# Kernel tuning notes

Hardware: AMD Instinct MI355X
Metric: run time of the kernel (lower is better)

The kernel has to match this reference:

```python
import jax, jax.numpy as jnp
import numpy as np

N = 50000      # nodes
E = 800000     # edges
F_IN = 128     # input_dim
H = 4          # GAT heads
C = 32         # hidden_dim (per head)
HC = H * C     # 128, concat GAT output
NG = 64        # graphs in batch
OUT = 10       # classes


def _gat_conv(x, src, dst, W, att_src, att_dst, bias):
    # PyG GATConv (concat=True, add_self_loops=True, negative_slope=0.2)
    n = x.shape[0]
    h = (x @ W).reshape(n, H, -1)                      # [N,H,C]
    a_s = (h * att_src).sum(-1)                        # [N,H]
    a_d = (h * att_dst).sum(-1)                        # [N,H]
    loop = jnp.arange(n)
    s = jnp.concatenate([src, loop])                   # self-loops appended
    d = jnp.concatenate([dst, loop])
    e = jax.nn.leaky_relu(a_s[s] + a_d[d], 0.2)        # [E+N,H]
    m = jax.ops.segment_max(e, d, num_segments=n)
    e = jnp.exp(e - m[d])
    z = jax.ops.segment_sum(e, d, num_segments=n)
    alpha = e / (z[d] + 1e-16)                         # edge softmax per dst,head
    out = jax.ops.segment_sum(h[s] * alpha[..., None], d, num_segments=n)
    return out.reshape(n, -1) + bias                   # [N,H*C]


def setup_inputs() -> dict:
    key = jax.random.key(0)
    ks = jax.random.split(key, 20)
    g = lambda k, shp, fan: jax.random.normal(k, shp, jnp.float32) / np.sqrt(fan)
    inp = {
        'x': jax.random.normal(ks[0], (N, F_IN), jnp.float32),
        'edge_index': jax.random.randint(ks[1], (2, E), 0, N),
        'batch': jnp.sort(jax.random.randint(ks[2], (N,), 0, NG)),
        # GATConv 1: F_IN -> H*C
        'W1': g(ks[3], (F_IN, HC), F_IN),
        'as1': g(ks[4], (H, C), C), 'ad1': g(ks[5], (H, C), C),
        'b1': jnp.zeros((HC,), jnp.float32),
        # GATConv 2: H*C -> H*C
        'W2': g(ks[6], (HC, HC), HC),
        'as2': g(ks[7], (H, C), C), 'ad2': g(ks[8], (H, C), C),
        'b2': jnp.zeros((HC,), jnp.float32),
        # GraphConv: H*C -> C  (lin_rel has bias, lin_root does not)
        'W3r': g(ks[9], (HC, C), HC), 'W3l': g(ks[10], (HC, C), HC),
        'b3': jnp.zeros((C,), jnp.float32),
        # SAGEConv: C -> C (mean aggr; lin_l has bias, lin_r does not)
        'W4l': g(ks[11], (C, C), C), 'b4l': jnp.zeros((C,), jnp.float32),
        'W4r': g(ks[12], (C, C), C),
        # MLP head
        'Wf1': g(ks[13], (C, C), C), 'bf1': jnp.zeros((C,), jnp.float32),
        'Wf2': g(ks[14], (C, OUT), C), 'bf2': jnp.zeros((OUT,), jnp.float32),
    }
    return inp


def reference(x, edge_index, batch, W1, as1, ad1, b1, W2, as2, ad2, b2,
              W3r, W3l, b3, W4l, b4l, W4r, Wf1, bf1, Wf2, bf2):
    src, dst = edge_index[0], edge_index[1]
    relu = jax.nn.relu
    n = x.shape[0]
    # GAT layers (dropout is identity in eval)
    x = relu(_gat_conv(x, src, dst, W1, as1, ad1, b1))
    x = relu(_gat_conv(x, src, dst, W2, as2, ad2, b2))
    # GraphConv: lin_rel(sum_neighbors) + lin_root(x)
    agg = jax.ops.segment_sum(x[src], dst, num_segments=n)
    x = relu(agg @ W3r + b3 + x @ W3l)
    # SAGEConv: lin_l(mean_neighbors) + lin_r(x)
    deg = jax.ops.segment_sum(jnp.ones((src.shape[0],), x.dtype), dst, num_segments=n)
    mean = jax.ops.segment_sum(x[src], dst, num_segments=n) / jnp.maximum(deg, 1.0)[:, None]
    x = relu(mean @ W4l + b4l + x @ W4r)
    # global mean pool over graphs
    cnt = jax.ops.segment_sum(jnp.ones((n,), x.dtype), batch, num_segments=NG)
    gpool = jax.ops.segment_sum(x, batch, num_segments=NG) / jnp.maximum(cnt, 1.0)[:, None]
    gpool = relu(gpool @ Wf1 + bf1)
    return gpool @ Wf2 + bf2
```

## Files before the change

kernel.cpp:

```cpp
#include <hip/hip_runtime.h>
#include <hip/hip_bf16.h>
#include <type_traits>


typedef __bf16 v8bf __attribute__((ext_vector_type(8)));
typedef float  v4f  __attribute__((ext_vector_type(4)));
typedef float  v2f  __attribute__((ext_vector_type(2)));

__device__ __forceinline__ float lrelu(float x) { return x > 0.f ? x : 0.2f * x; }

__device__ __forceinline__ unsigned short f2bf(float f) {
    unsigned u = __float_as_uint(f);
    unsigned r = (u + 0x7FFF + ((u >> 16) & 1)) >> 16;
    return (unsigned short)r;
}
__device__ __forceinline__ float bfbits2f(unsigned short u) {
    return __uint_as_float((unsigned)u << 16);
}
__device__ __forceinline__ float bflo(int v) { return __uint_as_float((unsigned)v << 16); }
__device__ __forceinline__ float bfhi(int v) { return __uint_as_float((unsigned)v & 0xffff0000u); }
__device__ __forceinline__ v2f up2(int v) {
    v2f r; r.x = bflo(v); r.y = bfhi(v); return r;
}
__device__ __forceinline__ int packbf2(float a, float b) {
    return (int)f2bf(a) | ((int)f2bf(b) << 16);
}


__global__ __launch_bounds__(256) void bucket_hist(const int* __restrict__ dst,
                                                   int* __restrict__ bcount,
                                                   int E, int nbuck) {
    __shared__ int hist[256];
    int t = threadIdx.x;
    for (int i = t; i < nbuck; i += 256) hist[i] = 0;
    __syncthreads();
    int base = blockIdx.x * 4096;
    #pragma unroll
    for (int k = 0; k < 16; ++k) {
        int e = base + k * 256 + t;
        if (e < E) atomicAdd(&hist[dst[e] >> 8], 1);
    }
    __syncthreads();
    for (int i = t; i < nbuck; i += 256) {
        int c = hist[i];
        if (c) atomicAdd(&bcount[i], c);
    }
}

__global__ __launch_bounds__(256) void scan_convert(
    const int* __restrict__ bcount, int* __restrict__ bbase, int* __restrict__ gcursor,
    int nbuck, int E, int* __restrict__ rowptr, int n,
    const float* __restrict__ W1, const float* __restrict__ W2,
    const float* __restrict__ W3r, const float* __restrict__ W3l,
    const float* __restrict__ as1, const float* __restrict__ ad1,
    const float* __restrict__ as2, const float* __restrict__ ad2,
    __hip_bfloat16* __restrict__ W1t, __hip_bfloat16* __restrict__ W2t,
    __hip_bfloat16* __restrict__ W3rt, __hip_bfloat16* __restrict__ W3lt)
{
    int t = threadIdx.x;
    if (blockIdx.x == 0) {
        __shared__ int red[256];
        int v = (t < nbuck) ? bcount[t] : 0;
        red[t] = v;
        __syncthreads();
        for (int off = 1; off < 256; off <<= 1) {
            int u = (t >= off) ? red[t - off] : 0;
            __syncthreads();
            red[t] += u;
            __syncthreads();
        }
        int ex = red[t] - v;
        if (t < nbuck) { bbase[t] = ex; gcursor[t] = ex; }
        if (t == 0) { bbase[nbuck] = E; rowptr[n] = E; }
        return;
    }
    int b = blockIdx.x - 1;
    int i = b * 256 + t;
    {
        int k = i >> 7, c = i & 127;
        *(unsigned short*)&W1t[c * 128 + k] = f2bf(W1[i]);
        *(unsigned short*)&W2t[c * 128 + k] = f2bf(W2[i]);
    }
    if (i < 4096) {
        int k = i >> 5, c = i & 31;
        *(unsigned short*)&W3rt[c * 128 + k] = f2bf(W3r[i]);
        *(unsigned short*)&W3lt[c * 128 + k] = f2bf(W3l[i]);
    }
    if (b == 0) {
        for (int u = t; u < 512; u += 256) {
            int k = u & 127, hd = u >> 7;
            float vs1 = 0.f, vd1 = 0.f, vs2 = 0.f, vd2 = 0.f;
            #pragma unroll
            for (int j = 0; j < 32; ++j) {
                int c = hd * 32 + j;
                float w1 = W1[k * 128 + c], w2 = W2[k * 128 + c];
                vs1 += w1 * as1[c]; vd1 += w1 * ad1[c];
                vs2 += w2 * as2[c]; vd2 += w2 * ad2[c];
            }
            unsigned short h1s = f2bf(vs1), h1d = f2bf(vd1);
            unsigned short h2s = f2bf(vs2), h2d = f2bf(vd2);
            *(unsigned short*)&W1t[(128 + hd) * 128 + k] = h1s;
            *(unsigned short*)&W1t[(132 + hd) * 128 + k] = f2bf(vs1 - bfbits2f(h1s));
            *(unsigned short*)&W1t[(136 + hd) * 128 + k] = h1d;
            *(unsigned short*)&W1t[(140 + hd) * 128 + k] = f2bf(vd1 - bfbits2f(h1d));
            *(unsigned short*)&W2t[(128 + hd) * 128 + k] = h2s;
            *(unsigned short*)&W2t[(132 + hd) * 128 + k] = f2bf(vs2 - bfbits2f(h2s));
            *(unsigned short*)&W2t[(136 + hd) * 128 + k] = h2d;
            *(unsigned short*)&W2t[(140 + hd) * 128 + k] = f2bf(vd2 - bfbits2f(h2d));
        }
    }
}

__global__ __launch_bounds__(256) void bucket_scatter(const int* __restrict__ dst,
                                                      const int* __restrict__ src,
                                                      int* __restrict__ gcursor,
                                                      int* __restrict__ pairs,
                                                      int E, int nbuck) {
    __shared__ int hist[256], lcur[256];
    int t = threadIdx.x;
    for (int i = t; i < nbuck; i += 256) hist[i] = 0;
    __syncthreads();
    int base = blockIdx.x * 2048;
    int dreg[8];
    #pragma unroll
    for (int k = 0; k < 8; ++k) {
        int e = base + k * 256 + t;
        int d = (e < E) ? dst[e] : -1;
        dreg[k] = d;
        if (d >= 0) atomicAdd(&hist[d >> 8], 1);
    }
    __syncthreads();
    for (int i = t; i < nbuck; i += 256) {
        int c = hist[i];
        lcur[i] = c ? atomicAdd(&gcursor[i], c) : 0;
    }
    __syncthreads();
    #pragma unroll
    for (int k = 0; k < 8; ++k) {
        int e = base + k * 256 + t;
        if (e < E) {
            int d = dreg[k];
            int p = atomicAdd(&lcur[d >> 8], 1);
            pairs[p] = ((d & 255) << 17) | src[e];
        }
    }
}

__global__ __launch_bounds__(256) void bucket_fill(const int* __restrict__ pairs,
                                                   const int* __restrict__ bbase,
                                                   int* __restrict__ rowptr,
                                                   int* __restrict__ colsrc, int n) {
    __shared__ int deg[256], excl[256], cur[256];
    int b = blockIdx.x, t = threadIdx.x;
    int e0 = bbase[b], e1 = bbase[b + 1];
    int d0 = b << 8;
    deg[t] = 0;
    __syncthreads();
    for (int j = e0 + t; j < e1; j += 256)
        atomicAdd(&deg[pairs[j] >> 17], 1);
    __syncthreads();
    int v = deg[t];
    excl[t] = v;
    __syncthreads();
    for (int off = 1; off < 256; off <<= 1) {
        int u = (t >= off) ? excl[t - off] : 0;
        __syncthreads();
        excl[t] += u;
        __syncthreads();
    }
    int base = e0 + excl[t] - v;
    if (d0 + t < n) rowptr[d0 + t] = base;
    cur[t] = base;
    __syncthreads();
    for (int j = e0 + t; j < e1; j += 256) {
        int w = pairs[j];
        int p = atomicAdd(&cur[w >> 17], 1);
        colsrc[p] = w & 0x1FFFF;
    }
}

template <typename T>
__global__ __launch_bounds__(256) void gemm_att_mfma(
    const T* __restrict__ X, const __hip_bfloat16* __restrict__ Wt,
    __hip_bfloat16* __restrict__ h, float* __restrict__ a_s, float* __restrict__ a_d, int n)
{
    __shared__ __align__(16) __hip_bfloat16 sWt[144 * 136];
    int t = threadIdx.x;
    for (int i = t; i < 144 * 16; i += 256) {
        int row = i >> 4, ch = i & 15;
        *(int4*)&sWt[row * 136 + ch * 8] = *(const int4*)&Wt[row * 128 + ch * 8];
    }
    __syncthreads();
    int wave = t >> 6, lane = t & 63, quad = lane >> 4, l16 = lane & 15;
    int rowbase = (blockIdx.x * 4 + wave) * 16;
    if (rowbase >= n) return;

    v8bf z;
    #pragma unroll
    for (int i = 0; i < 8; ++i) z[i] = (__bf16)0.f;
    int arow = rowbase + l16;
    bool ok = arow < n;
    v8bf af[4];
    if constexpr (std::is_same<T, float>::value) {
        const float* xf = X + (size_t)(ok ? arow : 0) * 128;
        #pragma unroll
        for (int ks = 0; ks < 4; ++ks) {
            if (ok) {
                float4 u = *(const float4*)&xf[ks * 32 + quad * 8];
                float4 v = *(const float4*)&xf[ks * 32 + quad * 8 + 4];
                v8bf a;
                unsigned short r;
                r = f2bf(u.x); a[0] = *(__bf16*)&r;
                r = f2bf(u.y); a[1] = *(__bf16*)&r;
                r = f2bf(u.z); a[2] = *(__bf16*)&r;
                r = f2bf(u.w); a[3] = *(__bf16*)&r;
                r = f2bf(v.x); a[4] = *(__bf16*)&r;
                r = f2bf(v.y); a[5] = *(__bf16*)&r;
                r = f2bf(v.z); a[6] = *(__bf16*)&r;
                r = f2bf(v.w); a[7] = *(__bf16*)&r;
                af[ks] = a;
            } else af[ks] = z;
        }
    } else {
        const v8bf* px = (const v8bf*)(X + (size_t)(ok ? arow : 0) * 128);
        #pragma unroll
        for (int ks = 0; ks < 4; ++ks) af[ks] = ok ? px[ks * 4 + quad] : z;
    }

    v4f acc[9];
    #pragma unroll
    for (int ct = 0; ct < 9; ++ct) acc[ct] = (v4f){0.f, 0.f, 0.f, 0.f};
    #pragma unroll
    for (int ct = 0; ct < 9; ++ct) {
        #pragma unroll
        for (int ks = 0; ks < 4; ++ks) {
            v8bf b = *(const v8bf*)&sWt[(ct * 16 + l16) * 136 + ks * 32 + quad * 8];
            acc[ct] = __builtin_amdgcn_mfma_f32_16x16x32_bf16(af[ks], b, acc[ct], 0, 0, 0);
        }
    }

    #pragma unroll
    for (int reg = 0; reg < 4; ++reg) {
        int r = rowbase + quad * 4 + reg;
        if (r < n) {
            #pragma unroll
            for (int ct = 0; ct < 8; ++ct)
                *(unsigned short*)&h[(size_t)r * 128 + ct * 16 + l16] = f2bf(acc[ct][reg]);
        }
    }
    #pragma unroll
    for (int reg = 0; reg < 4; ++reg) {
        float v = acc[8][reg] + __shfl_xor(acc[8][reg], 4);
        int r = rowbase + quad * 4 + reg;
        if (r < n) {
            if (l16 < 4)                    a_s[r * 4 + l16] = v;
            else if (l16 >= 8 && l16 < 12)  a_d[r * 4 + (l16 - 8)] = v;
        }
    }
}

__global__ __launch_bounds__(256) void gat_aggr(
    const __hip_bfloat16* __restrict__ h, const float* __restrict__ a_s,
    const float* __restrict__ a_d,
    const int* __restrict__ rowptr, const int* __restrict__ colsrc,
    const float* __restrict__ bias, __hip_bfloat16* __restrict__ out, int n)
{
    __shared__ float s_w[4][64 * 4];
    int t = threadIdx.x;
    int wave = t >> 6, lane = t & 63;
    int d = blockIdx.x * 4 + wave;
    if (d >= n) d = n - 1;
    int beg = rowptr[d], end = rowptr[d + 1];
    int cnt = end - beg;
    float4 ad4 = *(const float4*)&a_d[d * 4];
    float4 asd = *(const float4*)&a_s[d * 4];
    float es0 = lrelu(asd.x + ad4.x), es1 = lrelu(asd.y + ad4.y);
    float es2 = lrelu(asd.z + ad4.z), es3 = lrelu(asd.w + ad4.w);
    float z0 = 0.f, z1 = 0.f, z2 = 0.f, z3 = 0.f;

    int l16 = lane & 15, egrp = lane >> 4;
    unsigned ch2 = (unsigned)(l16 * 16);
    int head = l16 >> 2;
    v2f a2[4];
    #pragma unroll
    for (int i = 0; i < 4; ++i) a2[i] = (v2f){0.f, 0.f};

    for (int j0 = 0; j0 < cnt; j0 += 64) {
        int ne = min(64, cnt - j0);
        float w0 = 0.f, w1 = 0.f, w2 = 0.f, w3 = 0.f;
        int s = 0;
        if (lane < ne) {
            s = colsrc[beg + j0 + lane];
            float4 sv = *(const float4*)&a_s[s * 4];
            w0 = __expf(lrelu(sv.x + ad4.x));
            w1 = __expf(lrelu(sv.y + ad4.y));
            w2 = __expf(lrelu(sv.z + ad4.z));
            w3 = __expf(lrelu(sv.w + ad4.w));
        }
        z0 += w0; z1 += w1; z2 += w2; z3 += w3;
        float4 wv = {w0, w1, w2, w3};
        *(float4*)&s_w[wave][lane * 4] = wv;
        __asm volatile("s_waitcnt lgkmcnt(0)" ::: "memory");
        int kmax = (ne + 3) >> 2;
        #pragma unroll 2
        for (int k = 0; k < kmax; ++k) {
            int j = egrp + 4 * k;
            int ss = __shfl(s, j);
            float wj = s_w[wave][j * 4 + head];
            v2f w2v = {wj, wj};
            unsigned off = ((unsigned)ss << 8) + ch2;
            int4 u = *(const int4*)((const char*)h + off);
            a2[0] += w2v * up2(u.x);
            a2[1] += w2v * up2(u.y);
            a2[2] += w2v * up2(u.z);
            a2[3] += w2v * up2(u.w);
        }
    }
    float acc[8] = {a2[0].x, a2[0].y, a2[1].x, a2[1].y,
                    a2[2].x, a2[2].y, a2[3].x, a2[3].y};
    #pragma unroll
    for (int off = 1; off < 64; off <<= 1) {
        z0 += __shfl_xor(z0, off);
        z1 += __shfl_xor(z1, off);
        z2 += __shfl_xor(z2, off);
        z3 += __shfl_xor(z3, off);
    }
    #pragma unroll
    for (int off = 16; off < 64; off <<= 1)
        #pragma unroll
        for (int i = 0; i < 8; ++i) acc[i] += __shfl_xor(acc[i], off);

    if (egrp == 0) {
        int ch = l16 * 8;
        float zh = (head < 2) ? (head == 0 ? z0 : z1) : (head == 2 ? z2 : z3);
        float eh = (head < 2) ? (head == 0 ? es0 : es1) : (head == 2 ? es2 : es3);
        float ws = __expf(eh);
        float inv = 1.f / (zh + ws + 1e-16f);
        int4 hu = *(const int4*)&h[(size_t)d * 128 + ch];
        float hs[8] = {bflo(hu.x), bfhi(hu.x), bflo(hu.y), bfhi(hu.y),
                       bflo(hu.z), bfhi(hu.z), bflo(hu.w), bfhi(hu.w)};
        float4 b0 = *(const float4*)&bias[ch];
        float4 b1 = *(const float4*)&bias[ch + 4];
        float o[8];
        o[0] = fmaxf((acc[0] + ws * hs[0]) * inv + b0.x, 0.f);
        o[1] = fmaxf((acc[1] + ws * hs[1]) * inv + b0.y, 0.f);
        o[2] = fmaxf((acc[2] + ws * hs[2]) * inv + b0.z, 0.f);
        o[3] = fmaxf((acc[3] + ws * hs[3]) * inv + b0.w, 0.f);
        o[4] = fmaxf((acc[4] + ws * hs[4]) * inv + b1.x, 0.f);
        o[5] = fmaxf((acc[5] + ws * hs[5]) * inv + b1.y, 0.f);
        o[6] = fmaxf((acc[6] + ws * hs[6]) * inv + b1.z, 0.f);
        o[7] = fmaxf((acc[7] + ws * hs[7]) * inv + b1.w, 0.f);
        int4 ou;
        ou.x = packbf2(o[0], o[1]); ou.y = packbf2(o[2], o[3]);
        ou.z = packbf2(o[4], o[5]); ou.w = packbf2(o[6], o[7]);
        *(int4*)&out[(size_t)d * 128 + ch] = ou;
    }
}

__global__ __launch_bounds__(256) void graphconv_lin(
    const __hip_bfloat16* __restrict__ Xb,
    const __hip_bfloat16* __restrict__ Wrt, const __hip_bfloat16* __restrict__ Wlt,
    const float* __restrict__ bias, __hip_bfloat16* __restrict__ y,
    float* __restrict__ root, int n)
{
    __shared__ __align__(16) __hip_bfloat16 sWr[32 * 136], sWl[32 * 136];
    int t = threadIdx.x;
    for (int i = t; i < 32 * 16; i += 256) {
        int row = i >> 4, ch = i & 15;
        *(int4*)&sWr[row * 136 + ch * 8] = *(const int4*)&Wrt[row * 128 + ch * 8];
        *(int4*)&sWl[row * 136 + ch * 8] = *(const int4*)&Wlt[row * 128 + ch * 8];
    }
    __syncthreads();
    int wave = t >> 6, lane = t & 63, quad = lane >> 4, l16 = lane & 15;
    int rowbase = (blockIdx.x * 4 + wave) * 16;
    if (rowbase >= n) return;

    v8bf z;
    #pragma unroll
    for (int i = 0; i < 8; ++i) z[i] = (__bf16)0.f;
    int arow = rowbase + l16;
    bool ok = arow < n;
    const v8bf* px = (const v8bf*)(Xb + (size_t)(ok ? arow : 0) * 128);
    v8bf fx[4];
    #pragma unroll
    for (int ks = 0; ks < 4; ++ks) fx[ks] = ok ? px[ks * 4 + quad] : z;

    v4f accR[2], accL[2];
    #pragma unroll
    for (int ct = 0; ct < 2; ++ct) {
        accR[ct] = (v4f){0.f, 0.f, 0.f, 0.f};
        accL[ct] = (v4f){0.f, 0.f, 0.f, 0.f};
        #pragma unroll
        for (int ks = 0; ks < 4; ++ks) {
            v8bf br = *(const v8bf*)&sWr[(ct * 16 + l16) * 136 + ks * 32 + quad * 8];
            accR[ct] = __builtin_amdgcn_mfma_f32_16x16x32_bf16(fx[ks], br, accR[ct], 0, 0, 0);
            v8bf bl = *(const v8bf*)&sWl[(ct * 16 + l16) * 136 + ks * 32 + quad * 8];
            accL[ct] = __builtin_amdgcn_mfma_f32_16x16x32_bf16(fx[ks], bl, accL[ct], 0, 0, 0);
        }
    }
    #pragma unroll
    for (int ct = 0; ct < 2; ++ct) {
        float bcol = bias[ct * 16 + l16];
        #pragma unroll
        for (int reg = 0; reg < 4; ++reg) {
            int r = rowbase + quad * 4 + reg;
            if (r < n) {
                *(unsigned short*)&y[(size_t)r * 32 + ct * 16 + l16] = f2bf(accR[ct][reg]);
                root[(size_t)r * 32 + ct * 16 + l16] = accL[ct][reg] + bcol;
            }
        }
    }
}

__global__ __launch_bounds__(256) void graphconv_aggr(
    const __hip_bfloat16* __restrict__ y, const float* __restrict__ root,
    const int* __restrict__ rowptr, const int* __restrict__ colsrc,
    __hip_bfloat16* __restrict__ x3, int n)
{
    int t = threadIdx.x;
    int wave = t >> 6, lane = t & 63;
    int d = blockIdx.x * 4 + wave;
    if (d >= n) d = n - 1;
    int beg = rowptr[d], end = rowptr[d + 1];
    int cnt = end - beg;
    int l4 = lane & 3, egrp = lane >> 2;
    unsigned ch2 = (unsigned)(l4 * 16);
    v2f a2[4];
    #pragma unroll
    for (int i = 0; i < 4; ++i) a2[i] = (v2f){0.f, 0.f};
    for (int j0 = 0; j0 < cnt; j0 += 64) {
        int ne = min(64, cnt - j0);
        int s = (lane < ne) ? colsrc[beg + j0 + lane] : 0;
        int kmax = (ne + 15) >> 4;
        #pragma unroll 2
        for (int k = 0; k < kmax; ++k) {
            int j = egrp + 16 * k;
            int ss = __shfl(s, j);
            float m = (j < ne) ? 1.f : 0.f;
            v2f m2 = {m, m};
            unsigned off = ((unsigned)ss << 6) + ch2;
            int4 u = *(const int4*)((const char*)y + off);
            a2[0] += m2 * up2(u.x);
            a2[1] += m2 * up2(u.y);
            a2[2] += m2 * up2(u.z);
            a2[3] += m2 * up2(u.w);
        }
    }
    float acc[8] = {a2[0].x, a2[0].y, a2[1].x, a2[1].y,
                    a2[2].x, a2[2].y, a2[3].x, a2[3].y};
    #pragma unroll
    for (int off = 4; off < 64; off <<= 1)
        #pragma unroll
        for (int i = 0; i < 8; ++i) acc[i] += __shfl_xor(acc[i], off);
    if (egrp == 0) {
        int ch = l4 * 8;
        float4 r0 = *(const float4*)&root[(size_t)d * 32 + ch];
        float4 r1 = *(const float4*)&root[(size_t)d * 32 + ch + 4];
        float o[8];
        o[0] = fmaxf(acc[0] + r0.x, 0.f); o[1] = fmaxf(acc[1] + r0.y, 0.f);
        o[2] = fmaxf(acc[2] + r0.z, 0.f); o[3] = fmaxf(acc[3] + r0.w, 0.f);
        o[4] = fmaxf(acc[4] + r1.x, 0.f); o[5] = fmaxf(acc[5] + r1.y, 0.f);
        o[6] = fmaxf(acc[6] + r1.z, 0.f); o[7] = fmaxf(acc[7] + r1.w, 0.f);
        int4 ou;
        ou.x = packbf2(o[0], o[1]); ou.y = packbf2(o[2], o[3]);
        ou.z = packbf2(o[4], o[5]); ou.w = packbf2(o[6], o[7]);
        *(int4*)&x3[(size_t)d * 32 + ch] = ou;
    }
}

__global__ __launch_bounds__(256) void sage_fused(
    const __hip_bfloat16* __restrict__ x3, const int* __restrict__ rowptr,
    const int* __restrict__ colsrc,
    const float* __restrict__ W4l, const float* __restrict__ b4l,
    const float* __restrict__ W4r, float* __restrict__ out, int n)
{
    __shared__ __align__(16) float sWl[32 * 32], sWr[32 * 32];
    __shared__ float s_mean[4][32], s_x3[4][32];
    int t = threadIdx.x;
    for (int i = t; i < 1024; i += 256) { sWl[i] = W4l[i]; sWr[i] = W4r[i]; }
    __syncthreads();

    int wave = t >> 6, lane = t & 63;
    int d = blockIdx.x * 4 + wave;
    if (d >= n) d = n - 1;
    int beg = rowptr[d], end = rowptr[d + 1];
    int cnt = end - beg;
    int l4 = lane & 3, egrp = lane >> 2;
    unsigned ch2 = (unsigned)(l4 * 16);
    v2f a2[4];
    #pragma unroll
    for (int i = 0; i < 4; ++i) a2[i] = (v2f){0.f, 0.f};
    for (int j0 = 0; j0 < cnt; j0 += 64) {
        int ne = min(64, cnt - j0);
        int s = (lane < ne) ? colsrc[beg + j0 + lane] : 0;
        int kmax = (ne + 15) >> 4;
        #pragma unroll 2
        for (int k = 0; k < kmax; ++k) {
            int j = egrp + 16 * k;
            int ss = __shfl(s, j);
            float m = (j < ne) ? 1.f : 0.f;
            v2f m2 = {m, m};
            unsigned off = ((unsigned)ss << 6) + ch2;
            int4 u = *(const int4*)((const char*)x3 + off);
            a2[0] += m2 * up2(u.x);
            a2[1] += m2 * up2(u.y);
            a2[2] += m2 * up2(u.z);
            a2[3] += m2 * up2(u.w);
        }
    }
    float acc[8] = {a2[0].x, a2[0].y, a2[1].x, a2[1].y,
                    a2[2].x, a2[2].y, a2[3].x, a2[3].y};
    #pragma unroll
    for (int off = 4; off < 64; off <<= 1)
        #pragma unroll
        for (int i = 0; i < 8; ++i) acc[i] += __shfl_xor(acc[i], off);
    if (egrp == 0) {
        int ch = l4 * 8;
        float invd = 1.f / fmaxf((float)cnt, 1.f);
        int4 xr = *(const int4*)&x3[(size_t)d * 32 + ch];
        #pragma unroll
        for (int i = 0; i < 8; ++i) s_mean[wave][ch + i] = acc[i] * invd;
        s_x3[wave][ch + 0] = bflo(xr.x); s_x3[wave][ch + 1] = bfhi(xr.x);
        s_x3[wave][ch + 2] = bflo(xr.y); s_x3[wave][ch + 3] = bfhi(xr.y);
        s_x3[wave][ch + 4] = bflo(xr.z); s_x3[wave][ch + 5] = bfhi(xr.z);
        s_x3[wave][ch + 6] = bflo(xr.w); s_x3[wave][ch + 7] = bfhi(xr.w);
    }
    __asm volatile("s_waitcnt lgkmcnt(0)" ::: "memory");
    int c = lane & 31, half = lane >> 5;
    const float* sm = &s_mean[wave][half * 16];
    const float* sx = &s_x3[wave][half * 16];
    float acc2 = 0.f;
    #pragma unroll
    for (int k = 0; k < 16; ++k) {
        int kk = half * 16 + k;
        acc2 += sm[k] * sWl[kk * 32 + c] + sx[k] * sWr[kk * 32 + c];
    }
    acc2 += __shfl_xor(acc2, 32);
    if (half == 0 && d < n)
        out[(size_t)d * 32 + c] = fmaxf(acc2 + b4l[c], 0.f);
}

__device__ __forceinline__ int lower_bound_i(const int* a, int n, int key) {
    int lo = 0, hi = n;
    while (lo < hi) { int mid = (lo + hi) >> 1; if (a[mid] < key) lo = mid + 1; else hi = mid; }
    return lo;
}

__global__ __launch_bounds__(256) void pool_kernel(
    const float* __restrict__ x, const int* __restrict__ batch,
    float* __restrict__ gpool, int n)
{
    int g = blockIdx.x;
    int lo = lower_bound_i(batch, n, g);
    int hi = lower_bound_i(batch, n, g + 1);
    int t = threadIdx.x;
    int c = t & 31, rr = t >> 5;
    float acc = 0.f;
    for (int i = lo + rr; i < hi; i += 8) acc += x[i * 32 + c];
    __shared__ float sred[256];
    sred[t] = acc;
    __syncthreads();
    if (t < 128) sred[t] += sred[t + 128];
    __syncthreads();
    if (t < 64) sred[t] += sred[t + 64];
    __syncthreads();
    if (t < 32) {
        float v = sred[t] + sred[t + 32];
        gpool[g * 32 + t] = v / fmaxf((float)(hi - lo), 1.f);
    }
}

__global__ __launch_bounds__(256) void head_kernel(
    const float* __restrict__ gpool, const float* __restrict__ Wf1, const float* __restrict__ bf1,
    const float* __restrict__ Wf2, const float* __restrict__ bf2, float* __restrict__ out)
{
    __shared__ float sg[64 * 32], st[64 * 32];
    __shared__ float sW1[32 * 32], sW2[32 * 10];
    int t = threadIdx.x;
    for (int i = t; i < 2048; i += 256) sg[i] = gpool[i];
    for (int i = t; i < 1024; i += 256) sW1[i] = Wf1[i];
    for (int i = t; i < 320; i += 256) sW2[i] = Wf2[i];
    __syncthreads();
    for (int i = t; i < 2048; i += 256) {
        int g = i >> 5, c = i & 31;
        float acc = bf1[c];
        #pragma unroll
        for (int k = 0; k < 32; ++k) acc += sg[g * 32 + k] * sW1[k * 32 + c];
        st[i] = fmaxf(acc, 0.f);
    }
    __syncthreads();
    for (int i = t; i < 640; i += 256) {
        int g = i / 10, o = i - g * 10;
        float acc = bf2[o];
        #pragma unroll
        for (int k = 0; k < 32; ++k) acc += st[g * 32 + k] * sW2[k * 10 + o];
        out[i] = acc;
    }
}

extern "C" void kernel_launch(void* const* d_in, const int* in_sizes, int n_in,
                              void* d_out, int out_size, void* d_ws, size_t ws_size,
                              hipStream_t stream) {
    const float* x    = (const float*)d_in[0];
    const int*   ei   = (const int*)d_in[1];
    const int*   batch= (const int*)d_in[2];
    const float* W1   = (const float*)d_in[3];
    const float* as1  = (const float*)d_in[4];
    const float* ad1  = (const float*)d_in[5];
    const float* b1   = (const float*)d_in[6];
    const float* W2   = (const float*)d_in[7];
    const float* as2  = (const float*)d_in[8];
    const float* ad2  = (const float*)d_in[9];
    const float* b2   = (const float*)d_in[10];
    const float* W3r  = (const float*)d_in[11];
    const float* W3l  = (const float*)d_in[12];
    const float* b3   = (const float*)d_in[13];
    const float* W4l  = (const float*)d_in[14];
    const float* b4l  = (const float*)d_in[15];
    const float* W4r  = (const float*)d_in[16];
    const float* Wf1  = (const float*)d_in[17];
    const float* bf1  = (const float*)d_in[18];
    const float* Wf2  = (const float*)d_in[19];
    const float* bf2  = (const float*)d_in[20];

    const int N = in_sizes[0] / 128;
    const int E = in_sizes[1] / 2;
    const int* src = ei;
    const int* dst = ei + E;

    char* p = (char*)d_ws;
    auto alloc = [&](size_t bytes) -> void* {
        void* r = (void*)p;
        p += (bytes + 255) & ~(size_t)255;
        return r;
    };
    __hip_bfloat16* buf1 = (__hip_bfloat16*)alloc((size_t)N * 128 * 2);
    __hip_bfloat16* buf2 = (__hip_bfloat16*)alloc((size_t)N * 128 * 2);
    __hip_bfloat16* buf3 = (__hip_bfloat16*)alloc((size_t)N * 128 * 2);
    float* aS     = (float*)alloc((size_t)N * 4 * 4);
    float* aD     = (float*)alloc((size_t)N * 4 * 4);
    int*   rowptr = (int*)alloc((size_t)(N + 1) * 4);
    int*   colsrc = (int*)alloc((size_t)E * 4);
    int*   bcount = (int*)alloc(256 * 4);
    int*   bbase  = (int*)alloc(257 * 4);
    int*   gcursor= (int*)alloc(256 * 4);
    __hip_bfloat16* W1t  = (__hip_bfloat16*)alloc(144 * 128 * 2);
    __hip_bfloat16* W2t  = (__hip_bfloat16*)alloc(144 * 128 * 2);
    __hip_bfloat16* W3rt = (__hip_bfloat16*)alloc(32 * 128 * 2);
    __hip_bfloat16* W3lt = (__hip_bfloat16*)alloc(32 * 128 * 2);
    float* gpool  = (float*)alloc(64 * 32 * 4);

    __hip_bfloat16* X3b  = buf2;
    float*          X4   = (float*)buf1;
    __hip_bfloat16* Y32  = buf3;
    float*          ROOT = (float*)((char*)buf3 + (((size_t)N * 32 * 2 + 255) & ~(size_t)255));
    int*            pairs = (int*)buf3;

    const int nbuck = (N + 255) >> 8;

    hipMemsetAsync(bcount, 0, 256 * 4, stream);
    bucket_hist<<<(E + 4095) / 4096, 256, 0, stream>>>(dst, bcount, E, nbuck);
    scan_convert<<<65, 256, 0, stream>>>(bcount, bbase, gcursor, nbuck, E, rowptr, N,
                                         W1, W2, W3r, W3l, as1, ad1, as2, ad2,
                                         W1t, W2t, W3rt, W3lt);
    bucket_scatter<<<(E + 2047) / 2048, 256, 0, stream>>>(dst, src, gcursor, pairs, E, nbuck);
    bucket_fill<<<nbuck, 256, 0, stream>>>(pairs, bbase, rowptr, colsrc, N);

    const int gmm = (N + 63) / 64;
    const int gag = (N + 3) / 4;
    gemm_att_mfma<float><<<gmm, 256, 0, stream>>>(x, W1t, buf3, aS, aD, N);
    gat_aggr<<<gag, 256, 0, stream>>>(buf3, aS, aD, rowptr, colsrc, b1, buf2, N);
    gemm_att_mfma<__hip_bfloat16><<<gmm, 256, 0, stream>>>(buf2, W2t, buf3, aS, aD, N);
    gat_aggr<<<gag, 256, 0, stream>>>(buf3, aS, aD, rowptr, colsrc, b2, buf1, N);
    graphconv_lin<<<gmm, 256, 0, stream>>>(buf1, W3rt, W3lt, b3, Y32, ROOT, N);
    graphconv_aggr<<<gag, 256, 0, stream>>>(Y32, ROOT, rowptr, colsrc, X3b, N);
    sage_fused<<<gag, 256, 0, stream>>>(X3b, rowptr, colsrc, W4l, b4l, W4r, X4, N);
    pool_kernel<<<64, 256, 0, stream>>>(X4, batch, gpool, N);
    head_kernel<<<1, 256, 0, stream>>>(gpool, Wf1, bf1, Wf2, bf2, (float*)d_out);
}
```

Baseline: 360.7 us.

## Replace histogram+scan CSR build with fixed-capacity buckets and unroll GAT gather

After: 364.5 us. Within noise of the previous version (+1.1%).

```diff
diff --git a/kernel.cpp b/kernel.cpp
--- a/kernel.cpp
+++ b/kernel.cpp
@@ -6,6 +6,8 @@
 typedef __bf16 v8bf __attribute__((ext_vector_type(8)));
 typedef float  v4f  __attribute__((ext_vector_type(4)));
 typedef float  v2f  __attribute__((ext_vector_type(2)));
+
+#define BCAP 6144
 
 __device__ __forceinline__ float lrelu(float x) { return x > 0.f ? x : 0.2f * x; }
 
@@ -27,29 +29,8 @@
 }
 
 
-__global__ __launch_bounds__(256) void bucket_hist(const int* __restrict__ dst,
-                                                   int* __restrict__ bcount,
-                                                   int E, int nbuck) {
-    __shared__ int hist[256];
-    int t = threadIdx.x;
-    for (int i = t; i < nbuck; i += 256) hist[i] = 0;
-    __syncthreads();
-    int base = blockIdx.x * 4096;
-    #pragma unroll
-    for (int k = 0; k < 16; ++k) {
-        int e = base + k * 256 + t;
-        if (e < E) atomicAdd(&hist[dst[e] >> 8], 1);
-    }
-    __syncthreads();
-    for (int i = t; i < nbuck; i += 256) {
-        int c = hist[i];
-        if (c) atomicAdd(&bcount[i], c);
-    }
-}
-
-__global__ __launch_bounds__(256) void scan_convert(
-    const int* __restrict__ bcount, int* __restrict__ bbase, int* __restrict__ gcursor,
-    int nbuck, int E, int* __restrict__ rowptr, int n,
+__global__ __launch_bounds__(256) void prep_kernel(
+    int* __restrict__ gcursor,
     const float* __restrict__ W1, const float* __restrict__ W2,
     const float* __restrict__ W3r, const float* __restrict__ W3l,
     const float* __restrict__ as1, const float* __restrict__ ad1,
@@ -59,19 +40,7 @@
 {
     int t = threadIdx.x;
     if (blockIdx.x == 0) {
-        __shared__ int red[256];
-        int v = (t < nbuck) ? bcount[t] : 0;
-        red[t] = v;
-        __syncthreads();
-        for (int off = 1; off < 256; off <<= 1) {
-            int u = (t >= off) ? red[t - off] : 0;
-            __syncthreads();
-            red[t] += u;
-            __syncthreads();
-        }
-        int ex = red[t] - v;
-        if (t < nbuck) { bbase[t] = ex; gcursor[t] = ex; }
-        if (t == 0) { bbase[nbuck] = E; rowptr[n] = E; }
+        gcursor[t] = t * BCAP;
         return;
     }
     int b = blockIdx.x - 1;
@@ -147,12 +116,12 @@
 }
 
 __global__ __launch_bounds__(256) void bucket_fill(const int* __restrict__ pairs,
-                                                   const int* __restrict__ bbase,
-                                                   int* __restrict__ rowptr,
+                                                   const int* __restrict__ gcursor,
+                                                   int2* __restrict__ rowdeg,
                                                    int* __restrict__ colsrc, int n) {
     __shared__ int deg[256], excl[256], cur[256];
     int b = blockIdx.x, t = threadIdx.x;
-    int e0 = bbase[b], e1 = bbase[b + 1];
+    int e0 = b * BCAP, e1 = gcursor[b];
     int d0 = b << 8;
     deg[t] = 0;
     __syncthreads();
@@ -169,7 +138,7 @@
         __syncthreads();
     }
     int base = e0 + excl[t] - v;
-    if (d0 + t < n) rowptr[d0 + t] = base;
+    if (d0 + t < n) rowdeg[d0 + t] = make_int2(base, v);
     cur[t] = base;
     __syncthreads();
     for (int j = e0 + t; j < e1; j += 256) {
@@ -262,7 +231,7 @@
 __global__ __launch_bounds__(256) void gat_aggr(
     const __hip_bfloat16* __restrict__ h, const float* __restrict__ a_s,
     const float* __restrict__ a_d,
-    const int* __restrict__ rowptr, const int* __restrict__ colsrc,
+    const int2* __restrict__ rowdeg, const int* __restrict__ colsrc,
     const float* __restrict__ bias, __hip_bfloat16* __restrict__ out, int n)
 {
     __shared__ float s_w[4][64 * 4];
@@ -270,8 +239,8 @@
     int wave = t >> 6, lane = t & 63;
     int d = blockIdx.x * 4 + wave;
     if (d >= n) d = n - 1;
-    int beg = rowptr[d], end = rowptr[d + 1];
-    int cnt = end - beg;
+    int2 rd = rowdeg[d];
+    int beg = rd.x, cnt = rd.y;
     float4 ad4 = *(const float4*)&a_d[d * 4];
     float4 asd = *(const float4*)&a_s[d * 4];
     float es0 = lrelu(asd.x + ad4.x), es1 = lrelu(asd.y + ad4.y);
@@ -302,9 +271,32 @@
         *(float4*)&s_w[wave][lane * 4] = wv;
         __asm volatile("s_waitcnt lgkmcnt(0)" ::: "memory");
         int kmax = (ne + 3) >> 2;
-        #pragma unroll 2
-        for (int k = 0; k < kmax; ++k) {
-            int j = egrp + 4 * k;
+        int k0 = 0;
+        for (; k0 + 4 <= kmax; k0 += 4) {
+            int ssq[4]; float wq[4];
+            #pragma unroll
+            for (int q = 0; q < 4; ++q) {
+                int j = egrp + 4 * (k0 + q);
+                ssq[q] = __shfl(s, j);
+                wq[q] = s_w[wave][j * 4 + head];
+            }
+            int4 uq[4];
+            #pragma unroll
+            for (int q = 0; q < 4; ++q) {
+                unsigned off = ((unsigned)ssq[q] << 8) + ch2;
+                uq[q] = *(const int4*)((const char*)h + off);
+            }
+            #pragma unroll
+            for (int q = 0; q < 4; ++q) {
+                v2f w2v = {wq[q], wq[q]};
+                a2[0] += w2v * up2(uq[q].x);
+                a2[1] += w2v * up2(uq[q].y);
+                a2[2] += w2v * up2(uq[q].z);
+                a2[3] += w2v * up2(uq[q].w);
+            }
+        }
+        for (; k0 < kmax; ++k0) {
+            int j = egrp + 4 * k0;
             int ss = __shfl(s, j);
             float wj = s_w[wave][j * 4 + head];
             v2f w2v = {wj, wj};
@@ -414,15 +406,15 @@
 
 __global__ __launch_bounds__(256) void graphconv_aggr(
     const __hip_bfloat16* __restrict__ y, const float* __restrict__ root,
-    const int* __restrict__ rowptr, const int* __restrict__ colsrc,
+    const int2* __restrict__ rowdeg, const int* __restrict__ colsrc,
     __hip_bfloat16* __restrict__ x3, int n)
 {
     int t = threadIdx.x;
     int wave = t >> 6, lane = t & 63;
     int d = blockIdx.x * 4 + wave;
     if (d >= n) d = n - 1;
-    int beg = rowptr[d], end = rowptr[d + 1];
-    int cnt = end - beg;
+    int2 rd = rowdeg[d];
+    int beg = rd.x, cnt = rd.y;
     int l4 = lane & 3, egrp = lane >> 2;
     unsigned ch2 = (unsigned)(l4 * 16);
     v2f a2[4];
@@ -469,7 +461,7 @@
 }
 
 __global__ __launch_bounds__(256) void sage_fused(
-    const __hip_bfloat16* __restrict__ x3, const int* __restrict__ rowptr,
+    const __hip_bfloat16* __restrict__ x3, const int2* __restrict__ rowdeg,
     const int* __restrict__ colsrc,
     const float* __restrict__ W4l, const float* __restrict__ b4l,
     const float* __restrict__ W4r, float* __restrict__ out, int n)
@@ -483,8 +475,8 @@
     int wave = t >> 6, lane = t & 63;
     int d = blockIdx.x * 4 + wave;
     if (d >= n) d = n - 1;
-    int beg = rowptr[d], end = rowptr[d + 1];
-    int cnt = end - beg;
+    int2 rd = rowdeg[d];
+    int beg = rd.x, cnt = rd.y;
     int l4 = lane & 3, egrp = lane >> 2;
     unsigned ch2 = (unsigned)(l4 * 16);
     v2f a2[4];
@@ -634,15 +626,15 @@
         p += (bytes + 255) & ~(size_t)255;
         return r;
     };
+    const int nbuck = (N + 255) >> 8;
+
     __hip_bfloat16* buf1 = (__hip_bfloat16*)alloc((size_t)N * 128 * 2);
     __hip_bfloat16* buf2 = (__hip_bfloat16*)alloc((size_t)N * 128 * 2);
     __hip_bfloat16* buf3 = (__hip_bfloat16*)alloc((size_t)N * 128 * 2);
     float* aS     = (float*)alloc((size_t)N * 4 * 4);
     float* aD     = (float*)alloc((size_t)N * 4 * 4);
-    int*   rowptr = (int*)alloc((size_t)(N + 1) * 4);
-    int*   colsrc = (int*)alloc((size_t)E * 4);
-    int*   bcount = (int*)alloc(256 * 4);
-    int*   bbase  = (int*)alloc(257 * 4);
+    int2*  rowdeg = (int2*)alloc((size_t)N * 8);
+    int*   colsrc = (int*)alloc((size_t)nbuck * BCAP * 4);
     int*   gcursor= (int*)alloc(256 * 4);
     __hip_bfloat16* W1t  = (__hip_bfloat16*)alloc(144 * 128 * 2);
     __hip_bfloat16* W2t  = (__hip_bfloat16*)alloc(144 * 128 * 2);
@@ -656,25 +648,20 @@
     float*          ROOT = (float*)((char*)buf3 + (((size_t)N * 32 * 2 + 255) & ~(size_t)255));
     int*            pairs = (int*)buf3;
 
-    const int nbuck = (N + 255) >> 8;
-
-    hipMemsetAsync(bcount, 0, 256 * 4, stream);
-    bucket_hist<<<(E + 4095) / 4096, 256, 0, stream>>>(dst, bcount, E, nbuck);
-    scan_convert<<<65, 256, 0, stream>>>(bcount, bbase, gcursor, nbuck, E, rowptr, N,
-                                         W1, W2, W3r, W3l, as1, ad1, as2, ad2,
-                                         W1t, W2t, W3rt, W3lt);
+    prep_kernel<<<65, 256, 0, stream>>>(gcursor, W1, W2, W3r, W3l,
+                                        as1, ad1, as2, ad2, W1t, W2t, W3rt, W3lt);
     bucket_scatter<<<(E + 2047) / 2048, 256, 0, stream>>>(dst, src, gcursor, pairs, E, nbuck);
-    bucket_fill<<<nbuck, 256, 0, stream>>>(pairs, bbase, rowptr, colsrc, N);
+    bucket_fill<<<nbuck, 256, 0, stream>>>(pairs, gcursor, rowdeg, colsrc, N);
 
     const int gmm = (N + 63) / 64;
     const int gag = (N + 3) / 4;
     gemm_att_mfma<float><<<gmm, 256, 0, stream>>>(x, W1t, buf3, aS, aD, N);
-    gat_aggr<<<gag, 256, 0, stream>>>(buf3, aS, aD, rowptr, colsrc, b1, buf2, N);
+    gat_aggr<<<gag, 256, 0, stream>>>(buf3, aS, aD, rowdeg, colsrc, b1, buf2, N);
     gemm_att_mfma<__hip_bfloat16><<<gmm, 256, 0, stream>>>(buf2, W2t, buf3, aS, aD, N);
-    gat_aggr<<<gag, 256, 0, stream>>>(buf3, aS, aD, rowptr, colsrc, b2, buf1, N);
+    gat_aggr<<<gag, 256, 0, stream>>>(buf3, aS, aD, rowdeg, colsrc, b2, buf1, N);
     graphconv_lin<<<gmm, 256, 0, stream>>>(buf1, W3rt, W3lt, b3, Y32, ROOT, N);
-    graphconv_aggr<<<gag, 256, 0, stream>>>(Y32, ROOT, rowptr, colsrc, X3b, N);
-    sage_fused<<<gag, 256, 0, stream>>>(X3b, rowptr, colsrc, W4l, b4l, W4r, X4, N);
+    graphconv_aggr<<<gag, 256, 0, stream>>>(Y32, ROOT, rowdeg, colsrc, X3b, N);
+    sage_fused<<<gag, 256, 0, stream>>>(X3b, rowdeg, colsrc, W4l, b4l, W4r, X4, N);
     pool_kernel<<<64, 256, 0, stream>>>(X4, batch, gpool, N);
     head_kernel<<<1, 256, 0, stream>>>(gpool, Wf1, bf1, Wf2, bf2, (float*)d_out);
 }
```
